# Kernel optimization log

Measured on AMD Instinct MI355X. Metric: run time of the kernel, lower is better.

The kernel has to match this reference:

```python
import jax, jax.numpy as jnp
import numpy as np

# Body-part joint index groups, in the exact concat order of the torch forward:
# p1 torso, p1 left_hand, p1 left_leg, p1 right_hand, p1 right_leg, then same +25 for person 2.
_P1 = [
    [0, 1, 2, 3, 20],
    [8, 9, 10, 11, 23, 24],
    [16, 17, 18, 19],
    [4, 5, 6, 7, 21, 22],
    [12, 13, 14, 15],
]
PARTS = [np.array(g) for g in _P1] + [np.array(g) + 25 for g in _P1]


def setup_inputs() -> dict:
    key = jax.random.key(0)
    k_x, k_w1, k_w2 = jax.random.split(key, 3)
    N, C, T, V = 64, 256, 64, 50
    H = C // 16  # hidden width of the squeeze-excite MLP
    x = jax.random.normal(k_x, (N, C, T, V), dtype=jnp.float32)
    W1 = jax.random.normal(k_w1, (10, H, C), dtype=jnp.float32) * (2.0 / C) ** 0.5
    b1 = jnp.zeros((10, H), dtype=jnp.float32)
    W2 = jax.random.normal(k_w2, (10, C, H), dtype=jnp.float32) * (2.0 / H) ** 0.5
    b2 = jnp.zeros((10, C), dtype=jnp.float32)
    return {"x": x, "W1": W1, "b1": b1, "W2": W2, "b2": b2}


def reference(x, W1, b1, W2, b2):
    # x: [N, C, T, V=50]. For each of 10 fixed body parts: gather joints,
    # global avg & max pool over (T, joints), tiny 2-layer MLP on each pooled
    # vector, sigmoid(avg_path + max_path) channel gate, re-weight the slice.
    outs = []
    for p, idx in enumerate(PARTS):
        xs = x[:, :, :, idx]                       # [N, C, T, k]
        avg = jnp.mean(xs, axis=(2, 3))            # [N, C]
        mx = jnp.max(xs, axis=(2, 3))              # [N, C]

        def mlp(v):
            h = jax.nn.relu(v @ W1[p].T + b1[p])   # [N, H]
            return h @ W2[p].T + b2[p]             # [N, C]

        gate = jax.nn.sigmoid(mlp(avg) + mlp(mx))  # [N, C]
        outs.append(xs * gate[:, :, None, None])
    # Concatenate along the joint dim in part order (reorders joints, as in torch).
    return jnp.concatenate(outs, axis=3)           # [N, C, T, 50]
```

## Files before the change

### kernel.cpp

```cpp
#include <hip/hip_runtime.h>

#define N_  64
#define C_  256
#define T_  64
#define V_  50
#define H_  16
#define NP_ 10
#define ROW_ (T_ * V_)
#define NC_  (N_ * C_)
#define NPC_ (N_ * NP_ * C_)

typedef float f32x4 __attribute__((ext_vector_type(4)));

constexpr int PART_OF_V[V_] = {
    0,0,0,0, 3,3,3,3, 1,1,1,1, 4,4,4,4, 2,2,2,2, 0, 3,3, 1,1,
    5,5,5,5, 8,8,8,8, 6,6,6,6, 9,9,9,9, 7,7,7,7, 5, 8,8, 6,6};

__device__ const float INV_CNT_D[NP_] = {
    1.f/320, 1.f/384, 1.f/256, 1.f/384, 1.f/256,
    1.f/320, 1.f/384, 1.f/256, 1.f/384, 1.f/256};

__device__ const int SRC_V[V_] = {
    0,1,2,3,20,  8,9,10,11,23,24,  16,17,18,19,  4,5,6,7,21,22,  12,13,14,15,
    25,26,27,28,45,  33,34,35,36,48,49,  41,42,43,44,  29,30,31,32,46,47,  37,38,39,40};
__device__ const int PART_W[V_] = {
    0,0,0,0,0, 1,1,1,1,1,1, 2,2,2,2, 3,3,3,3,3,3, 4,4,4,4,
    5,5,5,5,5, 6,6,6,6,6,6, 7,7,7,7, 8,8,8,8,8,8, 9,9,9,9};

__global__ __launch_bounds__(256) void reduce_kernel(
    const float* __restrict__ x,
    float* __restrict__ avg_out,
    float* __restrict__ max_out) {
    __shared__ float lds[4][ROW_];
    const int wave = threadIdx.x >> 6;
    const int lane = threadIdx.x & 63;
    const int row  = blockIdx.x * 4 + wave;

    const float4* xr4 = (const float4*)(x + (size_t)row * ROW_);
    float4* l4 = (float4*)lds[wave];
    #pragma unroll
    for (int j = 0; j < 12; ++j) l4[lane + 64 * j] = xr4[lane + 64 * j];
    if (lane < 32) l4[lane + 768] = xr4[lane + 768];
    __syncthreads();

    const float2* l2 = (const float2*)(lds[wave] + lane * V_);
    float s[NP_], m[NP_];
    #pragma unroll
    for (int p = 0; p < NP_; ++p) { s[p] = 0.f; m[p] = -__builtin_huge_valf(); }
    #pragma unroll
    for (int j = 0; j < 25; ++j) {
        float2 q = l2[j];
        s[PART_OF_V[2*j]]   += q.x;
        m[PART_OF_V[2*j]]    = fmaxf(m[PART_OF_V[2*j]], q.x);
        s[PART_OF_V[2*j+1]] += q.y;
        m[PART_OF_V[2*j+1]]  = fmaxf(m[PART_OF_V[2*j+1]], q.y);
    }

    float* buf = lds[wave];
    #pragma unroll
    for (int p = 0; p < NP_; ++p) {
        buf[p * 66 + lane]          = s[p];
        buf[(p + 10) * 66 + lane]   = m[p];
    }
    __syncthreads();

    if (lane < 20) {
        const int n = row >> 8, c = row & 255;
        const float2* b2 = (const float2*)(lds[wave] + lane * 66);
        if (lane < 10) {
            float2 a = b2[0];
            float acc = a.x + a.y;
            #pragma unroll
            for (int j = 1; j < 32; ++j) { float2 q = b2[j]; acc += q.x + q.y; }
            avg_out[(n * NP_ + lane) * C_ + c] = acc * INV_CNT_D[lane];
        } else {
            const int p = lane - 10;
            float2 a = b2[0];
            float acc = fmaxf(a.x, a.y);
            #pragma unroll
            for (int j = 1; j < 32; ++j) { float2 q = b2[j]; acc = fmaxf(acc, fmaxf(q.x, q.y)); }
            max_out[(n * NP_ + p) * C_ + c] = acc;
        }
    }
}

__global__ __launch_bounds__(256) void mlp_kernel(
    const float* __restrict__ avg, const float* __restrict__ mx,
    const float* __restrict__ W1, const float* __restrict__ b1,
    const float* __restrict__ W2, const float* __restrict__ b2,
    float* __restrict__ gate) {
    const int np = blockIdx.x;
    const int p  = np % NP_;
    __shared__ float vec[2][C_];
    __shared__ float partial[256];
    __shared__ float hsum[H_];

    const int t = threadIdx.x;
    vec[0][t] = avg[np * C_ + t];
    vec[1][t] = mx[np * C_ + t];
    __syncthreads();

    const int which = t & 1, h = (t >> 1) & 15, chunk = t >> 5;
    const float* w1row = W1 + (p * H_ + h) * C_ + chunk * 32;
    const float* vv = vec[which] + chunk * 32;
    float acc = 0.f;
    #pragma unroll
    for (int k = 0; k < 32; ++k) acc += w1row[k] * vv[k];
    partial[t] = acc;
    __syncthreads();

    if (t < 32) {
        float a = b1[p * H_ + h];
        #pragma unroll
        for (int j = 0; j < 8; ++j) a += partial[t + 32 * j];
        a = fmaxf(a, 0.f);
        if (which == 0) hsum[h] = a;
    }
    __syncthreads();
    if (t < 32 && (t & 1) == 1) {
        float a = b1[p * H_ + h];
        #pragma unroll
        for (int j = 0; j < 8; ++j) a += partial[t + 32 * j];
        hsum[h] += fmaxf(a, 0.f);
    }
    __syncthreads();

    const float4* w2row = (const float4*)(W2 + (p * C_ + t) * H_);
    float z = 2.f * b2[p * C_ + t];
    #pragma unroll
    for (int q = 0; q < 4; ++q) {
        float4 w = w2row[q];
        z += w.x * hsum[4*q] + w.y * hsum[4*q+1] + w.z * hsum[4*q+2] + w.w * hsum[4*q+3];
    }
    gate[np * C_ + t] = 1.f / (1.f + __expf(-z));
}

__global__ __launch_bounds__(256) void scale_kernel(
    const float* __restrict__ x, const float* __restrict__ gate,
    float* __restrict__ out) {
    __shared__ float  lx[ROW_];
    __shared__ float4 tq[25];

    const int row = blockIdx.x;
    const int n = row >> 8, c = row & 255;
    const int tid = threadIdx.x;

    if (tid < V_) {
        const int w = tid;
        const float g = gate[(n * NP_ + PART_W[w]) * C_ + c];
        const int dsv = SRC_V[w] - w;
        float* t4 = (float*)&tq[w >> 1];
        t4[(w & 1) * 2 + 0] = __int_as_float(dsv);
        t4[(w & 1) * 2 + 1] = g;
    }

    const float4* src = (const float4*)(x + (size_t)row * ROW_);
    float4 d0 = src[tid];
    float4 d1 = src[tid + 256];
    float4 d2 = src[tid + 512];
    float4 d3 = {};
    if (tid < 32) d3 = src[tid + 768];

    {
        float vals[16] = {d0.x,d0.y,d0.z,d0.w, d1.x,d1.y,d1.z,d1.w,
                          d2.x,d2.y,d2.z,d2.w, d3.x,d3.y,d3.z,d3.w};
        #pragma unroll
        for (int r = 0; r < 4; ++r) {
            if (r == 3 && tid >= 32) break;
            const int f0 = (tid + 256 * r) * 4;
            #pragma unroll
            for (int k = 0; k < 4; ++k) {
                const int f = f0 + k;
                lx[f ^ ((f >> 5) & 3)] = vals[r * 4 + k];
            }
        }
    }
    __syncthreads();

    f32x4* dst = (f32x4*)(out + (size_t)row * ROW_);
    int w0 = (tid << 2) % 50u;
    #pragma unroll
    for (int rep = 0; rep < 4; ++rep) {
        if (rep == 3 && tid >= 32) break;
        const int u  = tid + 256 * rep;
        const int e0 = u * 4;
        int wB = w0 + 2; if (wB >= V_) wB -= V_;
        const float4 tA = tq[w0 >> 1];
        const float4 tB = tq[wB >> 1];
        const int f0 = e0 + 0 + __float_as_int(tA.x);
        const int f1 = e0 + 1 + __float_as_int(tA.z);
        const int f2 = e0 + 2 + __float_as_int(tB.x);
        const int f3 = e0 + 3 + __float_as_int(tB.z);
        f32x4 o;
        o.x = lx[f0 ^ ((f0 >> 5) & 3)] * tA.y;
        o.y = lx[f1 ^ ((f1 >> 5) & 3)] * tA.w;
        o.z = lx[f2 ^ ((f2 >> 5) & 3)] * tB.y;
        o.w = lx[f3 ^ ((f3 >> 5) & 3)] * tB.w;
        __builtin_nontemporal_store(o, &dst[u]);
        w0 += 24; if (w0 >= V_) w0 -= V_;
    }
}

extern "C" void kernel_launch(void* const* d_in, const int* in_sizes, int n_in,
                              void* d_out, int out_size, void* d_ws, size_t ws_size,
                              hipStream_t stream) {
    const float* x  = (const float*)d_in[0];
    const float* W1 = (const float*)d_in[1];
    const float* b1 = (const float*)d_in[2];
    const float* W2 = (const float*)d_in[3];
    const float* b2 = (const float*)d_in[4];
    float* out = (float*)d_out;

    float* avg  = (float*)d_ws;
    float* mx   = avg + NPC_;
    float* gate = mx + NPC_;

    reduce_kernel<<<NC_ / 4, 256, 0, stream>>>(x, avg, mx);
    mlp_kernel<<<N_ * NP_, 256, 0, stream>>>(avg, mx, W1, b1, W2, b2, gate);
    scale_kernel<<<NC_, 256, 0, stream>>>(x, gate, out);
}
```

Baseline: 386.8 us.

## Reduce directly from global by joint-aligned float4 lanes, drop full-row LDS staging

The reduce kernel no longer copies each 3200-float row into LDS. Each of 50 lanes reads float4s at stride 50 float4s, so a lane always covers the same four flattened positions modulo 200 and accumulates per-position sum and max over the 16 steps. A small LDS buffer then lets 20 lanes combine the per-part members through a membership table. This removes the large LDS footprint and the two-pass register scatter, which should raise occupancy, at the cost of 14 idle lanes per wave and a serial combine step.

```diff
diff --git a/kernel.cpp b/kernel.cpp
--- a/kernel.cpp
+++ b/kernel.cpp
@@ -12,13 +12,15 @@
 
 typedef float f32x4 __attribute__((ext_vector_type(4)));
 
-constexpr int PART_OF_V[V_] = {
-    0,0,0,0, 3,3,3,3, 1,1,1,1, 4,4,4,4, 2,2,2,2, 0, 3,3, 1,1,
-    5,5,5,5, 8,8,8,8, 6,6,6,6, 9,9,9,9, 7,7,7,7, 5, 8,8, 6,6};
-
 __device__ const float INV_CNT_D[NP_] = {
     1.f/320, 1.f/384, 1.f/256, 1.f/384, 1.f/256,
     1.f/320, 1.f/384, 1.f/256, 1.f/384, 1.f/256};
+
+__device__ const int MEMB[NP_][6] = {
+    { 0, 1, 2, 3,20,50}, { 8, 9,10,11,23,24}, {16,17,18,19,50,50},
+    { 4, 5, 6, 7,21,22}, {12,13,14,15,50,50},
+    {25,26,27,28,45,50}, {33,34,35,36,48,49}, {41,42,43,44,50,50},
+    {29,30,31,32,46,47}, {37,38,39,40,50,50}};
 
 __device__ const int SRC_V[V_] = {
     0,1,2,3,20,  8,9,10,11,23,24,  16,17,18,19,  4,5,6,7,21,22,  12,13,14,15,
@@ -31,56 +33,50 @@
     const float* __restrict__ x,
     float* __restrict__ avg_out,
     float* __restrict__ max_out) {
-    __shared__ float lds[4][ROW_];
+    __shared__ float sm[4][2][204];
     const int wave = threadIdx.x >> 6;
     const int lane = threadIdx.x & 63;
     const int row  = blockIdx.x * 4 + wave;
-
-    const float4* xr4 = (const float4*)(x + (size_t)row * ROW_);
-    float4* l4 = (float4*)lds[wave];
-    #pragma unroll
-    for (int j = 0; j < 12; ++j) l4[lane + 64 * j] = xr4[lane + 64 * j];
-    if (lane < 32) l4[lane + 768] = xr4[lane + 768];
-    __syncthreads();
-
-    const float2* l2 = (const float2*)(lds[wave] + lane * V_);
-    float s[NP_], m[NP_];
-    #pragma unroll
-    for (int p = 0; p < NP_; ++p) { s[p] = 0.f; m[p] = -__builtin_huge_valf(); }
-    #pragma unroll
-    for (int j = 0; j < 25; ++j) {
-        float2 q = l2[j];
-        s[PART_OF_V[2*j]]   += q.x;
-        m[PART_OF_V[2*j]]    = fmaxf(m[PART_OF_V[2*j]], q.x);
-        s[PART_OF_V[2*j+1]] += q.y;
-        m[PART_OF_V[2*j+1]]  = fmaxf(m[PART_OF_V[2*j+1]], q.y);
-    }
-
-    float* buf = lds[wave];
-    #pragma unroll
-    for (int p = 0; p < NP_; ++p) {
-        buf[p * 66 + lane]          = s[p];
-        buf[(p + 10) * 66 + lane]   = m[p];
+    const float NINF = -__builtin_huge_valf();
+
+    const float4* xr = (const float4*)(x + (size_t)row * ROW_);
+    if (lane < 50) {
+        float s0=0.f, s1=0.f, s2=0.f, s3=0.f;
+        float m0=NINF, m1=NINF, m2=NINF, m3=NINF;
+        #pragma unroll
+        for (int t = 0; t < 16; ++t) {
+            float4 d = xr[t * 50 + lane];
+            s0 += d.x; m0 = fmaxf(m0, d.x);
+            s1 += d.y; m1 = fmaxf(m1, d.y);
+            s2 += d.z; m2 = fmaxf(m2, d.z);
+            s3 += d.w; m3 = fmaxf(m3, d.w);
+        }
+        *(float4*)&sm[wave][0][4 * lane] = make_float4(s0, s1, s2, s3);
+        *(float4*)&sm[wave][1][4 * lane] = make_float4(m0, m1, m2, m3);
     }
     __syncthreads();
 
     if (lane < 20) {
+        const int p    = lane % 10;
+        const int kind = lane / 10;
+        const float* base = sm[wave][kind];
+        const float ident = kind ? NINF : 0.f;
+        float acc = ident;
+        #pragma unroll
+        for (int j = 0; j < 6; ++j) {
+            const int v  = MEMB[p][j];
+            const bool ok = (v < 50);
+            const int vv = ok ? v : 0;
+            #pragma unroll
+            for (int q = 0; q < 4; ++q) {
+                float val = base[vv + 50 * q];
+                val = ok ? val : ident;
+                acc = kind ? fmaxf(acc, val) : (acc + val);
+            }
+        }
         const int n = row >> 8, c = row & 255;
-        const float2* b2 = (const float2*)(lds[wave] + lane * 66);
-        if (lane < 10) {
-            float2 a = b2[0];
-            float acc = a.x + a.y;
-            #pragma unroll
-            for (int j = 1; j < 32; ++j) { float2 q = b2[j]; acc += q.x + q.y; }
-            avg_out[(n * NP_ + lane) * C_ + c] = acc * INV_CNT_D[lane];
-        } else {
-            const int p = lane - 10;
-            float2 a = b2[0];
-            float acc = fmaxf(a.x, a.y);
-            #pragma unroll
-            for (int j = 1; j < 32; ++j) { float2 q = b2[j]; acc = fmaxf(acc, fmaxf(q.x, q.y)); }
-            max_out[(n * NP_ + p) * C_ + c] = acc;
-        }
+        if (kind == 0) avg_out[(n * NP_ + p) * C_ + c] = acc * INV_CNT_D[p];
+        else           max_out[(n * NP_ + p) * C_ + c] = acc;
     }
 }
 
```

Result: no change. 387.1 us (+0.1%).
